# Kernel optimization log

Measured on AMD Instinct MI355X. Metric: run time of the kernel, lower is better.

Reference implementation:

```python
import jax, jax.numpy as jnp
import numpy as np

CHEB_K = 3  # from init_kwargs


def setup_inputs() -> dict:
    key = jax.random.key(0)
    k1, k2, k3, k4 = jax.random.split(key, 4)
    B, N, C_IN, C_OUT, D = 32, 4096, 32, 64, 16
    x = jax.random.normal(k1, (B, N, C_IN), dtype=jnp.float32)
    node_embeddings = jax.random.normal(k2, (N, D), dtype=jnp.float32)
    laplacian_mx = jnp.zeros((N, N), dtype=jnp.float32)  # unused by forward
    weights_pool = jax.random.normal(k3, (D, CHEB_K, C_IN, C_OUT), dtype=jnp.float32) * 0.1
    bias_pool = jax.random.normal(k4, (D, C_OUT), dtype=jnp.float32) * 0.1
    return {
        'x': x,
        'node_embeddings': node_embeddings,
        'laplacian_mx': laplacian_mx,
        'weights_pool': weights_pool,
        'bias_pool': bias_pool,
    }


def reference(x, node_embeddings, laplacian_mx, weights_pool, bias_pool):
    N = node_embeddings.shape[0]
    # adaptive adjacency: softmax(relu(E E^T)) over rows
    supports = jax.nn.softmax(jax.nn.relu(node_embeddings @ node_embeddings.T), axis=1)
    # Chebyshev recursion T_0=I, T_1=A, T_k = 2A T_{k-1} - T_{k-2}
    support_set = [jnp.eye(N, dtype=x.dtype), supports]
    for _ in range(2, CHEB_K):
        support_set.append(2.0 * supports @ support_set[-1] - support_set[-2])
    supports_k = jnp.stack(support_set, axis=0)  # [K, N, N]
    # per-node generated weights/bias
    weights = jnp.einsum('nd,dkio->nkio', node_embeddings, weights_pool)  # [N,K,I,O]
    bias = node_embeddings @ bias_pool  # [N, O]
    # graph propagation: [K,N,N] x [B,N,I] -> [B,K,N,I] -> [B,N,K,I]
    x_g = jnp.einsum('knm,bmc->bknc', supports_k, x).transpose(0, 2, 1, 3)
    # per-node grouped GEMM
    out = jnp.einsum('bnki,nkio->bno', x_g, weights) + bias
    return out
```

## Files before the change

### kernel.cpp

```cpp
#include <hip/hip_runtime.h>
#include <hip/hip_bf16.h>

#define N_NODES 4096
#define BATCH   32
#define CIN     32
#define COUT    64
#define DEMB    16
#define NCOL    (BATCH * CIN)
#define KIO     (3 * CIN * COUT)
#define SK1     3
#define SK2     4

typedef __bf16 bf16x8 __attribute__((ext_vector_type(8)));
typedef float  floatx4 __attribute__((ext_vector_type(4)));

__device__ inline void load_lds16(const void* g, void* l) {
    __builtin_amdgcn_global_load_lds(
        (const __attribute__((address_space(1))) void*)g,
        (__attribute__((address_space(3))) void*)l, 16, 0, 0);
}

__device__ __forceinline__ void compute_U_body(
        const float* __restrict__ E, __hip_bfloat16* __restrict__ U,
        float* __restrict__ invRow, int bx, int t) {
    const int n0   = bx * 8;
    const int lane = t & 63, wave = t >> 6;
    __shared__ float red[4][8];

    float en[8][DEMB];
#pragma unroll
    for (int r = 0; r < 8; ++r) {
        const float4* er = (const float4*)&E[(size_t)(n0 + r) * DEMB];
        const float4 a0 = er[0], a1 = er[1], a2 = er[2], a3 = er[3];
        en[r][ 0]=a0.x; en[r][ 1]=a0.y; en[r][ 2]=a0.z; en[r][ 3]=a0.w;
        en[r][ 4]=a1.x; en[r][ 5]=a1.y; en[r][ 6]=a1.z; en[r][ 7]=a1.w;
        en[r][ 8]=a2.x; en[r][ 9]=a2.y; en[r][10]=a2.z; en[r][11]=a2.w;
        en[r][12]=a3.x; en[r][13]=a3.y; en[r][14]=a3.z; en[r][15]=a3.w;
    }

    float sum[8] = {0.f, 0.f, 0.f, 0.f, 0.f, 0.f, 0.f, 0.f};

    for (int tile = 0; tile < 16; ++tile) {
        const int c = tile * 256 + t;
        const float4* em4 = (const float4*)&E[(size_t)c * DEMB];
        const float4 b0 = em4[0], b1 = em4[1], b2 = em4[2], b3 = em4[3];
        float em[DEMB];
        em[ 0]=b0.x; em[ 1]=b0.y; em[ 2]=b0.z; em[ 3]=b0.w;
        em[ 4]=b1.x; em[ 5]=b1.y; em[ 6]=b1.z; em[ 7]=b1.w;
        em[ 8]=b2.x; em[ 9]=b2.y; em[10]=b2.z; em[11]=b2.w;
        em[12]=b3.x; em[13]=b3.y; em[14]=b3.z; em[15]=b3.w;
#pragma unroll
        for (int r = 0; r < 8; ++r) {
            float dt = 0.f;
#pragma unroll
            for (int d = 0; d < DEMB; ++d) dt += en[r][d] * em[d];
            const float ev = __expf(fmaxf(dt, 0.f));
            sum[r] += ev;
            U[(size_t)(n0 + r) * N_NODES + c] = __float2bfloat16(ev);
        }
    }
#pragma unroll
    for (int r = 0; r < 8; ++r)
#pragma unroll
        for (int off = 32; off > 0; off >>= 1) sum[r] += __shfl_xor(sum[r], off);
    if (lane == 0)
#pragma unroll
        for (int r = 0; r < 8; ++r) red[wave][r] = sum[r];
    __syncthreads();
    if (t < 8)
        invRow[n0 + t] = 1.0f / (red[0][t] + red[1][t] + red[2][t] + red[3][t]);
}

__device__ __forceinline__ void transpose_body(
        const float* __restrict__ x,
        __hip_bfloat16* __restrict__ Xt, __hip_bfloat16* __restrict__ Bt,
        int m0, int b, int t) {
    __shared__ float tile[64][33];
    {
        const int ml = t >> 2, cg = (t & 3) * 8;
        const float* src = &x[((size_t)b * N_NODES + (m0 + ml)) * CIN + cg];
        const float4 r0 = *(const float4*)src;
        const float4 r1 = *(const float4*)(src + 4);
        tile[ml][cg+0] = r0.x; tile[ml][cg+1] = r0.y; tile[ml][cg+2] = r0.z; tile[ml][cg+3] = r0.w;
        tile[ml][cg+4] = r1.x; tile[ml][cg+5] = r1.y; tile[ml][cg+6] = r1.z; tile[ml][cg+7] = r1.w;
    }
    __syncthreads();
    {
        const int ml = t >> 2, cg = (t & 3) * 8;
        __hip_bfloat16* dst = &Xt[(size_t)(m0 + ml) * NCOL + b * CIN + cg];
#pragma unroll
        for (int j = 0; j < 8; ++j) dst[j] = __float2bfloat16(tile[ml][cg + j]);
    }
    {
        const int c = t >> 3, mg = (t & 7) * 8;
        __hip_bfloat16* dst = &Bt[(size_t)(b * CIN + c) * N_NODES + m0 + mg];
#pragma unroll
        for (int j = 0; j < 8; ++j) dst[j] = __float2bfloat16(tile[mg + j][c]);
    }
}

__global__ __launch_bounds__(256) void prep_kernel(
        const float* __restrict__ E, const float* __restrict__ x,
        __hip_bfloat16* __restrict__ U, float* __restrict__ invRow,
        __hip_bfloat16* __restrict__ Xt, __hip_bfloat16* __restrict__ Bt) {
    const int bx = blockIdx.x, t = threadIdx.x;
    if (bx < 512) {
        compute_U_body(E, U, invRow, bx, t);
    } else {
        const int idx = bx - 512;
        transpose_body(x, Xt, Bt, (idx & 63) << 6, idx >> 6, t);
    }
}

__global__ __launch_bounds__(256) void gen_w_kernel(
        const float* __restrict__ E, const float* __restrict__ Wp,
        __hip_bfloat16* __restrict__ Wn) {
    const int c   = blockIdx.x >> 3;
    const int oo0 = (blockIdx.x & 7) * 8;
    const int nc  = blockIdx.y * 64;
    const int t   = threadIdx.x;
    const int kk  = t & 31;
    const int oo  = oo0 + (t >> 5);

    __shared__ float et[64][DEMB];
    ((float4*)et)[t] = ((const float4*)&E[(size_t)nc * DEMB])[t];
    __syncthreads();

    const int srccol = (c * 32 + kk) * 64 + oo;
    float w[DEMB];
#pragma unroll
    for (int d = 0; d < DEMB; ++d) w[d] = Wp[(size_t)d * KIO + srccol];

    const int dstoff = c * 2048 + (oo >> 4) * 512 + (oo & 15) * 32 + kk;
    for (int nl = 0; nl < 64; ++nl) {
        float acc = 0.0f;
#pragma unroll
        for (int d = 0; d < DEMB; ++d) acc += et[nl][d] * w[d];
        Wn[(size_t)(nc + nl) * KIO + dstoff] = __float2bfloat16(acc);
    }
}

__global__ __launch_bounds__(256) void gemm128_kernel(
        const __hip_bfloat16* __restrict__ A,
        const __hip_bfloat16* __restrict__ Bt,
        __hip_bfloat16* __restrict__ P,
        int M, int NC, int K) {
    const int t    = threadIdx.x;
    const int row0 = blockIdx.x * 128;
    const int col0 = blockIdx.y * 128;
    const int z    = blockIdx.z;
    const int iters = K >> 6;
    const int q = iters / SK1, rem = iters % SK1;
    const int it0 = z * q + (z < rem ? z : rem);
    const int it1 = it0 + q + (z < rem ? 1 : 0);

    __shared__ alignas(16) __hip_bfloat16 As[128 * 64];
    __shared__ alignas(16) __hip_bfloat16 Bs[128 * 64];
    const int lane = t & 63, wave = t >> 6;
    const int l16 = lane & 15, quad = lane >> 4;
    const int wrow = (wave >> 1) * 64, wcol = (wave & 1) * 64;
    const int xr = l16 & 7;

    floatx4 acc[4][4] = {};

    for (int it = it0; it < it1; ++it) {
        const int kb = it << 6;
        __syncthreads();
#pragma unroll
        for (int s = 0; s < 4; ++s) {
            const int gi = s * 256 + t;
            const int r  = gi >> 3;
            const int cg = (gi & 7) ^ (r & 7);
            load_lds16(&A [(size_t)(row0 + r) * K + kb + cg * 8], &As[gi * 8]);
            load_lds16(&Bt[(size_t)(col0 + r) * K + kb + cg * 8], &Bs[gi * 8]);
        }
        __syncthreads();
#pragma unroll
        for (int ks = 0; ks < 2; ++ks) {
            bf16x8 af[4], bfr[4];
#pragma unroll
            for (int i = 0; i < 4; ++i)
                af[i]  = *(const bf16x8*)&As[(wrow + i * 16 + l16) * 64 +
                                             (((ks * 4 + quad) ^ xr) * 8)];
#pragma unroll
            for (int i = 0; i < 4; ++i)
                bfr[i] = *(const bf16x8*)&Bs[(wcol + i * 16 + l16) * 64 +
                                             (((ks * 4 + quad) ^ xr) * 8)];
#pragma unroll
            for (int i = 0; i < 4; ++i)
#pragma unroll
                for (int j = 0; j < 4; ++j)
                    acc[i][j] = __builtin_amdgcn_mfma_f32_16x16x32_bf16(
                                    af[i], bfr[j], acc[i][j], 0, 0, 0);
        }
    }

    __hip_bfloat16* Pz = P + (size_t)z * M * NC;
#pragma unroll
    for (int i = 0; i < 4; ++i)
#pragma unroll
        for (int j = 0; j < 4; ++j)
#pragma unroll
            for (int r = 0; r < 4; ++r) {
                const int rg = row0 + wrow + i * 16 + quad * 4 + r;
                const int cg = col0 + wcol + j * 16 + l16;
                Pz[(size_t)rg * NC + cg] = __float2bfloat16(acc[i][j][r]);
            }
}

#define GBM 256
#define GBN 256
#define GBK 64

__global__ __launch_bounds__(512, 2) void gemm256_pinned_kernel(
        const __hip_bfloat16* __restrict__ A,
        const __hip_bfloat16* __restrict__ Bt,
        __hip_bfloat16* __restrict__ P,
        int M, int NC, int K) {
    const int t    = threadIdx.x;
    const int row0 = blockIdx.x * GBM;
    const int col0 = blockIdx.y * GBN;
    const int z    = blockIdx.z;
    const int NT   = (K >> 6) / SK2;
    const int kb0  = z * NT * GBK;

    __shared__ alignas(16) __hip_bfloat16 As[2][16384];
    __shared__ alignas(16) __hip_bfloat16 Bs[2][16384];

    const int lane = t & 63, wave = t >> 6;
    const int l16 = lane & 15, quad = lane >> 4;
    const int wr = wave >> 2, wc = wave & 3;

    const int R0 = wr * 128 + l16;
    const int C0 = wc * 64 + l16;
    const int u_par = (l16 & 1) * 4 + quad;
    const int Aoff = (R0 >> 1) * 64 + ((u_par ^ ((R0 >> 1) & 7)) * 8);
    const int Boff = (C0 >> 1) * 64 + ((u_par ^ ((C0 >> 1) & 7)) * 8);

    auto stageA = [&](int buf, int kb, int kh, int s) {
        const int L = s * 512 + t;
        const int p = L >> 3, j = L & 7;
        const int u = j ^ (p & 7);
        const int rr = p * 2 + (u >> 2);
        const int qq = u & 3;
        load_lds16(&A[(size_t)(row0 + rr) * K + kb + kh * 32 + qq * 8],
                   &As[buf][(size_t)(kh * 1024 + L) * 8]);
    };
    auto stageB = [&](int buf, int kb, int kh, int s) {
        const int L = s * 512 + t;
        const int p = L >> 3, j = L & 7;
        const int u = j ^ (p & 7);
        const int rr = p * 2 + (u >> 2);
        const int qq = u & 3;
        load_lds16(&Bt[(size_t)(col0 + rr) * K + kb + kh * 32 + qq * 8],
                   &Bs[buf][(size_t)(kh * 1024 + L) * 8]);
    };

    floatx4 acc[8][4] = {};

#pragma unroll
    for (int s = 0; s < 2; ++s) stageA(0, kb0, 0, s);
#pragma unroll
    for (int s = 0; s < 2; ++s) stageB(0, kb0, 0, s);
#pragma unroll
    for (int s = 0; s < 2; ++s) stageA(0, kb0, 1, s);
#pragma unroll
    for (int s = 0; s < 2; ++s) stageB(0, kb0, 1, s);
#pragma unroll
    for (int s = 0; s < 2; ++s) stageA(1, kb0 + GBK, 0, s);
#pragma unroll
    for (int s = 0; s < 2; ++s) stageB(1, kb0 + GBK, 0, s);
    asm volatile("s_waitcnt vmcnt(4)" ::: "memory");
    __builtin_amdgcn_s_barrier();
    __builtin_amdgcn_sched_barrier(0);

    for (int tt = 0; tt < NT; ++tt) {
        const int buf = tt & 1;
        const int nb1 = (tt + 1) & 1;
        const int nb2 = buf;
        const int kb1 = kb0 + (tt + 1) * GBK;
        const int kb2 = kb0 + (tt + 2) * GBK;
        const bool g1 = (tt + 1 < NT), g2 = (tt + 2 < NT);

        bf16x8 bfrag[4], afrag[4];

#pragma unroll
        for (int n = 0; n < 4; ++n)
            bfrag[n] = *(const bf16x8*)&Bs[buf][n * 512 + Boff];
#pragma unroll
        for (int m = 0; m < 4; ++m)
            afrag[m] = *(const bf16x8*)&As[buf][m * 512 + Aoff];
        if (g1) { stageA(nb1, kb1, 1, 0); stageA(nb1, kb1, 1, 1); }
        __builtin_amdgcn_s_barrier();
        asm volatile("s_waitcnt lgkmcnt(0)" ::: "memory");
        __builtin_amdgcn_sched_barrier(0);
        __builtin_amdgcn_s_setprio(1);
#pragma unroll
        for (int m = 0; m < 4; ++m)
#pragma unroll
            for (int n = 0; n < 4; ++n)
                acc[m][n] = __builtin_amdgcn_mfma_f32_16x16x32_bf16(
                                afrag[m], bfrag[n], acc[m][n], 0, 0, 0);
        __builtin_amdgcn_s_setprio(0);
        __builtin_amdgcn_s_barrier();

#pragma unroll
        for (int m = 0; m < 4; ++m)
            afrag[m] = *(const bf16x8*)&As[buf][2048 + m * 512 + Aoff];
        if (g1) { stageB(nb1, kb1, 1, 0); stageB(nb1, kb1, 1, 1); }
        __builtin_amdgcn_s_barrier();
        asm volatile("s_waitcnt lgkmcnt(0)" ::: "memory");
        __builtin_amdgcn_sched_barrier(0);
        __builtin_amdgcn_s_setprio(1);
#pragma unroll
        for (int m = 0; m < 4; ++m)
#pragma unroll
            for (int n = 0; n < 4; ++n)
                acc[4 + m][n] = __builtin_amdgcn_mfma_f32_16x16x32_bf16(
                                    afrag[m], bfrag[n], acc[4 + m][n], 0, 0, 0);
        __builtin_amdgcn_s_setprio(0);
        __builtin_amdgcn_s_barrier();

#pragma unroll
        for (int n = 0; n < 4; ++n)
            bfrag[n] = *(const bf16x8*)&Bs[buf][8192 + n * 512 + Boff];
#pragma unroll
        for (int m = 0; m < 4; ++m)
            afrag[m] = *(const bf16x8*)&As[buf][8192 + m * 512 + Aoff];
        if (g2) { stageA(nb2, kb2, 0, 0); stageA(nb2, kb2, 0, 1); }
        __builtin_amdgcn_s_barrier();
        asm volatile("s_waitcnt lgkmcnt(0)" ::: "memory");
        __builtin_amdgcn_sched_barrier(0);
        __builtin_amdgcn_s_setprio(1);
#pragma unroll
        for (int m = 0; m < 4; ++m)
#pragma unroll
            for (int n = 0; n < 4; ++n)
                acc[m][n] = __builtin_amdgcn_mfma_f32_16x16x32_bf16(
                                afrag[m], bfrag[n], acc[m][n], 0, 0, 0);
        __builtin_amdgcn_s_setprio(0);
        __builtin_amdgcn_s_barrier();

#pragma unroll
        for (int m = 0; m < 4; ++m)
            afrag[m] = *(const bf16x8*)&As[buf][8192 + 2048 + m * 512 + Aoff];
        if (g2) { stageB(nb2, kb2, 0, 0); stageB(nb2, kb2, 0, 1); }
        __builtin_amdgcn_s_barrier();
        asm volatile("s_waitcnt lgkmcnt(0)" ::: "memory");
        __builtin_amdgcn_sched_barrier(0);
        __builtin_amdgcn_s_setprio(1);
#pragma unroll
        for (int m = 0; m < 4; ++m)
#pragma unroll
            for (int n = 0; n < 4; ++n)
                acc[4 + m][n] = __builtin_amdgcn_mfma_f32_16x16x32_bf16(
                                    afrag[m], bfrag[n], acc[4 + m][n], 0, 0, 0);
        __builtin_amdgcn_s_setprio(0);
        if (tt < NT - 2) asm volatile("s_waitcnt vmcnt(4)" ::: "memory");
        else             asm volatile("s_waitcnt vmcnt(0)" ::: "memory");
        __builtin_amdgcn_s_barrier();
        __builtin_amdgcn_sched_barrier(0);
    }

    __hip_bfloat16* Pz = P + (size_t)z * M * NC;
#pragma unroll
    for (int mq = 0; mq < 2; ++mq)
#pragma unroll
        for (int m = 0; m < 4; ++m)
#pragma unroll
            for (int n = 0; n < 4; ++n)
#pragma unroll
                for (int r = 0; r < 4; ++r) {
                    const int rg = row0 + wr * 128 + mq * 64 + m * 16 + quad * 4 + r;
                    const int cg = col0 + wc * 64 + n * 16 + l16;
                    Pz[(size_t)rg * NC + cg] = __float2bfloat16(acc[mq * 4 + m][n][r]);
                }
}

__global__ __launch_bounds__(256) void combine1_kernel(
        const __hip_bfloat16* __restrict__ P, const float* __restrict__ invRow,
        __hip_bfloat16* __restrict__ Y, __hip_bfloat16* __restrict__ Yt,
        int M, int NC) {
    const int c0 = blockIdx.x * 64, m0 = blockIdx.y * 64;
    const int t = threadIdx.x;
    __shared__ float tile[64][65];
    const size_t stride = (size_t)M * NC;
#pragma unroll
    for (int j = 0; j < 16; ++j) {
        const int lin = t + j * 256;
        const int r = lin >> 6, c = lin & 63;
        const size_t idx = (size_t)(m0 + r) * NC + c0 + c;
        float s = 0.f;
#pragma unroll
        for (int z = 0; z < SK1; ++z) s += __bfloat162float(P[idx + z * stride]);
        s *= invRow[m0 + r];
        tile[r][c] = s;
        Y[idx] = __float2bfloat16(s);
    }
    __syncthreads();
#pragma unroll
    for (int j = 0; j < 16; ++j) {
        const int lin = t + j * 256;
        const int c = lin >> 6, r = lin & 63;
        Yt[(size_t)(c0 + c) * M + m0 + r] = __float2bfloat16(tile[r][c]);
    }
}

__global__ __launch_bounds__(256) void final_kernel(
        const __hip_bfloat16* __restrict__ Xt, const __hip_bfloat16* __restrict__ Y1,
        const __hip_bfloat16* __restrict__ P,  const float* __restrict__ invRow,
        const __hip_bfloat16* __restrict__ Wn,
        const float* __restrict__ E, const float* __restrict__ bias_pool,
        float* __restrict__ out) {
    const int t    = threadIdx.x;
    const int lane = t & 63, wave = t >> 6;
    const int l16  = lane & 15, quad = lane >> 4;
    const int n0   = blockIdx.x * 4;
    const int n    = n0 + wave;

    __shared__ float ost[32][4][65];

    const __hip_bfloat16* Wnode = Wn + (size_t)n * KIO;
    const float inv = invRow[n];
    const size_t pstride = (size_t)N_NODES * NCOL;

    floatx4 acc[2][4] = {};

    bf16x8 afX[2], afY1[2], afY2[2];
#pragma unroll
    for (int mt = 0; mt < 2; ++mt) {
        const size_t fo = (size_t)n * NCOL + (mt * 16 + l16) * 32 + quad * 8;
        afX[mt]  = *(const bf16x8*)&Xt[fo];
        afY1[mt] = *(const bf16x8*)&Y1[fo];
        const bf16x8 p0 = *(const bf16x8*)&P[fo];
        const bf16x8 p1 = *(const bf16x8*)&P[fo + pstride];
        const bf16x8 p2 = *(const bf16x8*)&P[fo + 2 * pstride];
        const bf16x8 p3 = *(const bf16x8*)&P[fo + 3 * pstride];
#pragma unroll
        for (int j = 0; j < 8; ++j) {
            const float s = (float)p0[j] + (float)p1[j] + (float)p2[j] + (float)p3[j];
            afY2[mt][j] = (__bf16)(2.0f * inv * s - (float)afX[mt][j]);
        }
    }

    const bf16x8* afs[3] = {afX, afY1, afY2};
#pragma unroll
    for (int c = 0; c < 3; ++c) {
#pragma unroll
        for (int ot = 0; ot < 4; ++ot) {
            const bf16x8 bfr = *(const bf16x8*)&Wnode[(size_t)c * 2048 +
                                                      ot * 512 + l16 * 32 + quad * 8];
#pragma unroll
            for (int mt = 0; mt < 2; ++mt)
                acc[mt][ot] = __builtin_amdgcn_mfma_f32_16x16x32_bf16(
                                  afs[c][mt], bfr, acc[mt][ot], 0, 0, 0);
        }
    }

    float en[DEMB];
#pragma unroll
    for (int d = 0; d < DEMB; ++d) en[d] = E[(size_t)n * DEMB + d];
#pragma unroll
    for (int ot = 0; ot < 4; ++ot) {
        float bv = 0.f;
        const int o = ot * 16 + l16;
#pragma unroll
        for (int d = 0; d < DEMB; ++d) bv += en[d] * bias_pool[d * COUT + o];
#pragma unroll
        for (int mt = 0; mt < 2; ++mt)
#pragma unroll
            for (int r = 0; r < 4; ++r) {
                const int b = mt * 16 + quad * 4 + r;
                ost[b][wave][o] = acc[mt][ot][r] + bv;
            }
    }
    __syncthreads();

#pragma unroll
    for (int j = 0; j < 8; ++j) {
        const int c  = t + j * 256;
        const int b  = c >> 6;
        const int rm = c & 63;
        const int nl = rm >> 4, o4 = (rm & 15) * 4;
        float4 v;
        v.x = ost[b][nl][o4 + 0]; v.y = ost[b][nl][o4 + 1];
        v.z = ost[b][nl][o4 + 2]; v.w = ost[b][nl][o4 + 3];
        *(float4*)&out[((size_t)b * N_NODES + n0 + nl) * COUT + o4] = v;
    }
}

extern "C" void kernel_launch(void* const* d_in, const int* in_sizes, int n_in,
                              void* d_out, int out_size, void* d_ws, size_t ws_size,
                              hipStream_t stream) {
    (void)in_sizes; (void)n_in; (void)out_size; (void)ws_size;
    const float* x  = (const float*)d_in[0];
    const float* E  = (const float*)d_in[1];
    const float* Wp = (const float*)d_in[3];
    const float* bp = (const float*)d_in[4];
    float* out = (float*)d_out;

    char* ws = (char*)d_ws;
    __hip_bfloat16* U    = (__hip_bfloat16*)(ws);
    __hip_bfloat16* Bt1  = (__hip_bfloat16*)(ws + 33554432);
    __hip_bfloat16* Y1t  = (__hip_bfloat16*)(ws + 41943040);
    __hip_bfloat16* P    = (__hip_bfloat16*)(ws + 50331648);
    __hip_bfloat16* Y1   = (__hip_bfloat16*)(ws + 83886080);
    __hip_bfloat16* Xt   = (__hip_bfloat16*)(ws + 92274688);
    float*       invRow  = (float*)(ws + 100663296);
    __hip_bfloat16* Wn   = (__hip_bfloat16*)(ws);

    prep_kernel<<<2560, 256, 0, stream>>>(E, x, U, invRow, Xt, Bt1);
    gemm128_kernel<<<dim3(N_NODES / 128, NCOL / 128, SK1), 256, 0, stream>>>(
        U, Bt1, P, N_NODES, NCOL, N_NODES);
    combine1_kernel<<<dim3(NCOL / 64, N_NODES / 64), 256, 0, stream>>>(
        P, invRow, Y1, Y1t, N_NODES, NCOL);
    gemm256_pinned_kernel<<<dim3(N_NODES / GBM, NCOL / GBN, SK2), 512, 0, stream>>>(
        U, Y1t, P, N_NODES, NCOL, N_NODES);
    gen_w_kernel<<<dim3(24, N_NODES / 64), 256, 0, stream>>>(E, Wp, Wn);
    final_kernel<<<N_NODES / 4, 256, 0, stream>>>(Xt, Y1, P, invRow, Wn, E, bp, out);
}
```

Measured before the change: 281.8 us.

## Fuse per-node weight generation into final kernel via LDS

Removes the separate gen_w kernel, which wrote 4096x6144 bf16 per-node weights (~50MB) to global memory that the final kernel then read back. Each final_kernel block now generates the weights for its 4 nodes directly into padded LDS from weights_pool and the node embeddings, then feeds the MFMAs from LDS and reuses that buffer for output staging. The cost is that every block re-reads the whole weights_pool (16x6144 floats, served by cache) and does the embedding-dimension FMAs itself. It also adds more LDS use and extra barriers per block, which may lower occupancy.

```diff
diff --git a/kernel.cpp b/kernel.cpp
--- a/kernel.cpp
+++ b/kernel.cpp
@@ -12,6 +12,7 @@
 #define SK2     4
 
 typedef __bf16 bf16x8 __attribute__((ext_vector_type(8)));
+typedef __bf16 bf16x4 __attribute__((ext_vector_type(4)));
 typedef float  floatx4 __attribute__((ext_vector_type(4)));
 
 __device__ inline void load_lds16(const void* g, void* l) {
@@ -109,34 +110,6 @@
     } else {
         const int idx = bx - 512;
         transpose_body(x, Xt, Bt, (idx & 63) << 6, idx >> 6, t);
-    }
-}
-
-__global__ __launch_bounds__(256) void gen_w_kernel(
-        const float* __restrict__ E, const float* __restrict__ Wp,
-        __hip_bfloat16* __restrict__ Wn) {
-    const int c   = blockIdx.x >> 3;
-    const int oo0 = (blockIdx.x & 7) * 8;
-    const int nc  = blockIdx.y * 64;
-    const int t   = threadIdx.x;
-    const int kk  = t & 31;
-    const int oo  = oo0 + (t >> 5);
-
-    __shared__ float et[64][DEMB];
-    ((float4*)et)[t] = ((const float4*)&E[(size_t)nc * DEMB])[t];
-    __syncthreads();
-
-    const int srccol = (c * 32 + kk) * 64 + oo;
-    float w[DEMB];
-#pragma unroll
-    for (int d = 0; d < DEMB; ++d) w[d] = Wp[(size_t)d * KIO + srccol];
-
-    const int dstoff = c * 2048 + (oo >> 4) * 512 + (oo & 15) * 32 + kk;
-    for (int nl = 0; nl < 64; ++nl) {
-        float acc = 0.0f;
-#pragma unroll
-        for (int d = 0; d < DEMB; ++d) acc += et[nl][d] * w[d];
-        Wn[(size_t)(nc + nl) * KIO + dstoff] = __float2bfloat16(acc);
     }
 }
 
@@ -409,7 +382,7 @@
 __global__ __launch_bounds__(256) void final_kernel(
         const __hip_bfloat16* __restrict__ Xt, const __hip_bfloat16* __restrict__ Y1,
         const __hip_bfloat16* __restrict__ P,  const float* __restrict__ invRow,
-        const __hip_bfloat16* __restrict__ Wn,
+        const float* __restrict__ Wp,
         const float* __restrict__ E, const float* __restrict__ bias_pool,
         float* __restrict__ out) {
     const int t    = threadIdx.x;
@@ -418,13 +391,13 @@
     const int n0   = blockIdx.x * 4;
     const int n    = n0 + wave;
 
-    __shared__ float ost[32][4][65];
-
-    const __hip_bfloat16* Wnode = Wn + (size_t)n * KIO;
+    __shared__ alignas(16) __hip_bfloat16 WL[4 * 6912];
+    __shared__ float E4[4][16];
+
     const float inv = invRow[n];
     const size_t pstride = (size_t)N_NODES * NCOL;
 
-    floatx4 acc[2][4] = {};
+    if (t < 64) E4[t >> 4][t & 15] = E[(size_t)(n0 + (t >> 4)) * DEMB + (t & 15)];
 
     bf16x8 afX[2], afY1[2], afY2[2];
 #pragma unroll
@@ -442,36 +415,63 @@
             afY2[mt][j] = (__bf16)(2.0f * inv * s - (float)afX[mt][j]);
         }
     }
-
+    __syncthreads();
+
+#pragma unroll
+    for (int c = 0; c < 3; ++c)
+#pragma unroll
+        for (int p = 0; p < 8; ++p) {
+            const int kk = p * 4 + wave;
+            const int o  = lane;
+            const float* wp = &Wp[(size_t)(c * 32 + kk) * 64 + o];
+            float w[DEMB];
+#pragma unroll
+            for (int d = 0; d < DEMB; ++d) w[d] = wp[(size_t)d * KIO];
+            const int doff = c * 2304 + (o >> 4) * 576 + (o & 15) * 36 + kk;
+#pragma unroll
+            for (int nl = 0; nl < 4; ++nl) {
+                float a = 0.f;
+#pragma unroll
+                for (int d = 0; d < DEMB; ++d) a += E4[nl][d] * w[d];
+                WL[nl * 6912 + doff] = __float2bfloat16(a);
+            }
+        }
+    __syncthreads();
+
+    floatx4 acc[2][4] = {};
     const bf16x8* afs[3] = {afX, afY1, afY2};
+    const int wbase = wave * 6912;
 #pragma unroll
     for (int c = 0; c < 3; ++c) {
 #pragma unroll
         for (int ot = 0; ot < 4; ++ot) {
-            const bf16x8 bfr = *(const bf16x8*)&Wnode[(size_t)c * 2048 +
-                                                      ot * 512 + l16 * 32 + quad * 8];
+            const int be = wbase + c * 2304 + ot * 576 + l16 * 36 + quad * 8;
+            const bf16x4 lo = *(const bf16x4*)&WL[be];
+            const bf16x4 hi = *(const bf16x4*)&WL[be + 4];
+            bf16x8 bfr;
+#pragma unroll
+            for (int j = 0; j < 4; ++j) { bfr[j] = lo[j]; bfr[4 + j] = hi[j]; }
 #pragma unroll
             for (int mt = 0; mt < 2; ++mt)
                 acc[mt][ot] = __builtin_amdgcn_mfma_f32_16x16x32_bf16(
                                   afs[c][mt], bfr, acc[mt][ot], 0, 0, 0);
         }
     }
-
-    float en[DEMB];
-#pragma unroll
-    for (int d = 0; d < DEMB; ++d) en[d] = E[(size_t)n * DEMB + d];
+    __syncthreads();
+
+    float* ost = (float*)WL;
 #pragma unroll
     for (int ot = 0; ot < 4; ++ot) {
         float bv = 0.f;
         const int o = ot * 16 + l16;
 #pragma unroll
-        for (int d = 0; d < DEMB; ++d) bv += en[d] * bias_pool[d * COUT + o];
+        for (int d = 0; d < DEMB; ++d) bv += E4[wave][d] * bias_pool[d * COUT + o];
 #pragma unroll
         for (int mt = 0; mt < 2; ++mt)
 #pragma unroll
             for (int r = 0; r < 4; ++r) {
                 const int b = mt * 16 + quad * 4 + r;
-                ost[b][wave][o] = acc[mt][ot][r] + bv;
+                ost[(b * 4 + wave) * 65 + o] = acc[mt][ot][r] + bv;
             }
     }
     __syncthreads();
@@ -483,8 +483,8 @@
         const int rm = c & 63;
         const int nl = rm >> 4, o4 = (rm & 15) * 4;
         float4 v;
-        v.x = ost[b][nl][o4 + 0]; v.y = ost[b][nl][o4 + 1];
-        v.z = ost[b][nl][o4 + 2]; v.w = ost[b][nl][o4 + 3];
+        v.x = ost[(b * 4 + nl) * 65 + o4 + 0]; v.y = ost[(b * 4 + nl) * 65 + o4 + 1];
+        v.z = ost[(b * 4 + nl) * 65 + o4 + 2]; v.w = ost[(b * 4 + nl) * 65 + o4 + 3];
         *(float4*)&out[((size_t)b * N_NODES + n0 + nl) * COUT + o4] = v;
     }
 }
@@ -507,7 +507,6 @@
     __hip_bfloat16* Y1   = (__hip_bfloat16*)(ws + 83886080);
     __hip_bfloat16* Xt   = (__hip_bfloat16*)(ws + 92274688);
     float*       invRow  = (float*)(ws + 100663296);
-    __hip_bfloat16* Wn   = (__hip_bfloat16*)(ws);
 
     prep_kernel<<<2560, 256, 0, stream>>>(E, x, U, invRow, Xt, Bt1);
     gemm128_kernel<<<dim3(N_NODES / 128, NCOL / 128, SK1), 256, 0, stream>>>(
@@ -516,6 +515,6 @@
         P, invRow, Y1, Y1t, N_NODES, NCOL);
     gemm256_pinned_kernel<<<dim3(N_NODES / GBM, NCOL / GBN, SK2), 512, 0, stream>>>(
         U, Y1t, P, N_NODES, NCOL, N_NODES);
-    gen_w_kernel<<<dim3(24, N_NODES / 64), 256, 0, stream>>>(E, Wp, Wn);
-    final_kernel<<<N_NODES / 4, 256, 0, stream>>>(Xt, Y1, P, invRow, Wn, E, bp, out);
-}
+    final_kernel<<<N_NODES / 4, 256, 0, stream>>>(
+        Xt, Y1, P, invRow, Wp, E, bp, out);
+}
```

Result: slower. 296.3 us (+5.1%).
